# Performance work log

Measured on AMD Instinct MI355X. Metric: run time of the kernel, lower is better.

The kernel has to match this reference:

```python
import jax, jax.numpy as jnp
import numpy as np

B, L = 2, 1024
DIM = 512
N_LAYERS = 2
D_STATE = 16
D_CONV = 4
D_INNER = 2 * DIM          # expand_factor=2
DT_RANK = (DIM + 15) // 16  # ceil(d_model/16) = 32
VOCAB = 32000


def _rmsnorm(x, w, eps=1e-5):
    return x * jax.lax.rsqrt(jnp.mean(x * x, axis=-1, keepdims=True) + eps) * w


def _causal_conv(x, w, b):
    # x: (B,L,D_INNER); depthwise causal conv along L, kernel D_CONV
    xt = jnp.transpose(x, (0, 2, 1))  # (B,C,L)
    y = jax.lax.conv_general_dilated(
        xt, w, window_strides=(1,), padding=[(D_CONV - 1, 0)],
        dimension_numbers=('NCH', 'OIH', 'NCH'), feature_group_count=D_INNER)
    return jnp.transpose(y, (0, 2, 1)) + b


def _ssm(x, xproj_w, dt_w, dt_b, A_log, Dp):
    # x: (B,L,D_INNER)
    A = -jnp.exp(A_log)  # (D_INNER, D_STATE)
    dbc = jnp.einsum('bld,rd->blr', x, xproj_w)  # (B,L,DT_RANK+2*D_STATE)
    delta = jax.nn.softplus(jnp.einsum('blr,dr->bld', dbc[..., :DT_RANK], dt_w) + dt_b)
    Bm = dbc[..., DT_RANK:DT_RANK + D_STATE]   # (B,L,D_STATE)
    Cm = dbc[..., DT_RANK + D_STATE:]          # (B,L,D_STATE)
    dA = jnp.exp(delta[..., None] * A)                       # (B,L,D_INNER,D_STATE)
    dBx = (delta * x)[..., None] * Bm[:, :, None, :]         # (B,L,D_INNER,D_STATE)

    def step(h, inp):
        a, b = inp
        h = a * h + b
        return h, h

    h0 = jnp.zeros((x.shape[0], D_INNER, D_STATE), x.dtype)
    _, hs = jax.lax.scan(step, h0, (jnp.swapaxes(dA, 0, 1), jnp.swapaxes(dBx, 0, 1)))
    y = jnp.einsum('lbds,bls->bld', hs, Cm) + Dp * x
    return y


def _block(h, rw, iw, cw, cb, xw, dw, db, Al, Dp, ow):
    r = _rmsnorm(h, rw)
    xz = jnp.einsum('bld,ed->ble', r, iw)  # (B,L,2*D_INNER)
    xin, z = jnp.split(xz, 2, axis=-1)
    xin = jax.nn.silu(_causal_conv(xin, cw, cb))
    y = _ssm(xin, xw, dw, db, Al, Dp) * jax.nn.silu(z)
    return h + jnp.einsum('ble,de->bld', y, ow)


def _forward(x, embed, rms_w, in_w, conv_w, conv_b, xproj_w, dt_w, dt_b, A_log, Dp, out_w, ln_g, ln_b, head_w, head_b):
    h = embed[x]  # (B,L,DIM)
    for l in range(N_LAYERS):
        h = _block(h, rms_w[l], in_w[l], conv_w[l], conv_b[l], xproj_w[l],
                   dt_w[l], dt_b[l], A_log[l], Dp[l], out_w[l])
    mu = jnp.mean(h, axis=-1, keepdims=True)
    var = jnp.mean((h - mu) ** 2, axis=-1, keepdims=True)
    hn = (h - mu) * jax.lax.rsqrt(var + 1e-5) * ln_g + ln_b
    return jnp.einsum('bld,vd->blv', hn, head_w) + head_b


def setup_inputs() -> dict:
    key = jax.random.key(0)
    ks = jax.random.split(key, 10)
    s = 0.02
    x = jax.random.randint(ks[0], (B, L), 0, VOCAB)
    embed = jax.random.normal(ks[1], (VOCAB, DIM), jnp.float32) * s
    rms_w = jnp.ones((N_LAYERS, DIM), jnp.float32)
    in_w = jax.random.normal(ks[2], (N_LAYERS, 2 * D_INNER, DIM), jnp.float32) * s
    conv_w = jax.random.normal(ks[3], (N_LAYERS, D_INNER, 1, D_CONV), jnp.float32) * s
    conv_b = jnp.zeros((N_LAYERS, D_INNER), jnp.float32)
    xproj_w = jax.random.normal(ks[4], (N_LAYERS, DT_RANK + 2 * D_STATE, D_INNER), jnp.float32) * s
    dt_w = jax.random.normal(ks[5], (N_LAYERS, D_INNER, DT_RANK), jnp.float32) * s
    dt_b = jax.random.normal(ks[6], (N_LAYERS, D_INNER), jnp.float32) * s
    A_log = jnp.log(jnp.broadcast_to(jnp.arange(1, D_STATE + 1, dtype=jnp.float32), (N_LAYERS, D_INNER, D_STATE)))
    Dp = jnp.ones((N_LAYERS, D_INNER), jnp.float32)
    out_w = jax.random.normal(ks[7], (N_LAYERS, DIM, D_INNER), jnp.float32) * s
    ln_g = jnp.ones((DIM,), jnp.float32)
    ln_b = jnp.zeros((DIM,), jnp.float32)
    head_w = jax.random.normal(ks[8], (VOCAB, DIM), jnp.float32) * s
    head_b = jnp.zeros((VOCAB,), jnp.float32)
    return dict(x=x, embed=embed, rms_w=rms_w, in_w=in_w, conv_w=conv_w, conv_b=conv_b,
                xproj_w=xproj_w, dt_w=dt_w, dt_b=dt_b, A_log=A_log, Dp=Dp, out_w=out_w,
                ln_g=ln_g, ln_b=ln_b, head_w=head_w, head_b=head_b)


def reference(x, embed, rms_w, in_w, conv_w, conv_b, xproj_w, dt_w, dt_b, A_log, Dp, out_w, ln_g, ln_b, head_w, head_b):
    return _forward(x, embed, rms_w, in_w, conv_w, conv_b, xproj_w, dt_w, dt_b,
                    A_log, Dp, out_w, ln_g, ln_b, head_w, head_b)
```

## Files before the change

kernel.cpp:

```cpp
#include <hip/hip_runtime.h>

typedef unsigned short u16;
typedef __attribute__((ext_vector_type(8))) __bf16 bf16x8;
typedef __attribute__((ext_vector_type(4))) float f32x4;

#define B_ 2
#define L_ 1024
#define DIM_ 512
#define DINNER_ 1024
#define DSTATE_ 16
#define DTRANK_ 32
#define VOCAB_ 32000
#define NCHUNK 64
#define CLEN 16

__device__ __forceinline__ u16 f2bf(float f) {
    union { float f; unsigned u; } x; x.f = f;
    unsigned r = x.u + 0x7FFFu + ((x.u >> 16) & 1u);
    return (u16)(r >> 16);
}

__global__ __launch_bounds__(256) void prep(const float* __restrict__ in_w,
                                            const float* __restrict__ out_w,
                                            const float* __restrict__ head_w,
                                            const float* __restrict__ dt_w,
                                            const int* __restrict__ x,
                                            const float* __restrict__ embed,
                                            const float* __restrict__ rw,
                                            u16* __restrict__ win,
                                            u16* __restrict__ wout,
                                            u16* __restrict__ whd,
                                            float* __restrict__ dtwT,
                                            float* __restrict__ h,
                                            u16* __restrict__ rbf) {
    int bk = blockIdx.x;
    int t = threadIdx.x;
    if (bk < 19072) {
        const int n1 = 524288;
        const int n2 = n1 + 262144;
        int i = bk * 256 + t;
        const float4* s; ushort4* d; int j;
        if (i < n1)      { s = (const float4*)in_w;   d = (ushort4*)win;  j = i; }
        else if (i < n2) { s = (const float4*)out_w;  d = (ushort4*)wout; j = i - n1; }
        else             { s = (const float4*)head_w; d = (ushort4*)whd;  j = i - n2; }
        float4 v = s[j];
        ushort4 o; o.x = f2bf(v.x); o.y = f2bf(v.y); o.z = f2bf(v.z); o.w = f2bf(v.w);
        d[j] = o;
    } else if (bk < 19328) {
        int bb = bk - 19072;
        int l = bb >> 7;
        int e = (bb & 127) * 256 + t;
        int r = e >> 10, d = e & 1023;
        dtwT[(size_t)l * 32768 + r * 1024 + d] = dt_w[(size_t)l * 32768 + d * 32 + r];
    } else {
        int wave = t >> 6, lane = t & 63;
        int row = (bk - 19328) * 4 + wave;
        int tok = x[row];
        const float4* s = (const float4*)(embed + (size_t)tok * DIM_);
        float4 v0 = s[lane], v1 = s[lane + 64];
        float4* hd = (float4*)(h + (size_t)row * DIM_);
        hd[lane] = v0;
        hd[lane + 64] = v1;
        float ss = v0.x*v0.x + v0.y*v0.y + v0.z*v0.z + v0.w*v0.w
                 + v1.x*v1.x + v1.y*v1.y + v1.z*v1.z + v1.w*v1.w;
        for (int m = 1; m < 64; m <<= 1) ss += __shfl_xor(ss, m);
        float rms = rsqrtf(ss * (1.0f / DIM_) + 1e-5f);
        const float4* w4 = (const float4*)rw;
        float4 w0 = w4[lane], w1 = w4[lane + 64];
        u16* o = rbf + (size_t)row * DIM_;
        ushort4 a, b;
        a.x = f2bf(v0.x * rms * w0.x); a.y = f2bf(v0.y * rms * w0.y);
        a.z = f2bf(v0.z * rms * w0.z); a.w = f2bf(v0.w * rms * w0.w);
        b.x = f2bf(v1.x * rms * w1.x); b.y = f2bf(v1.y * rms * w1.y);
        b.z = f2bf(v1.z * rms * w1.z); b.w = f2bf(v1.w * rms * w1.w);
        *(ushort4*)(o + lane * 4) = a;
        *(ushort4*)(o + 256 + lane * 4) = b;
    }
}

__global__ __launch_bounds__(256) void rmsnorm_bf16(const float* __restrict__ h,
                                                    const float* __restrict__ w,
                                                    u16* __restrict__ out) {
    int wave = threadIdx.x >> 6, lane = threadIdx.x & 63;
    int row = blockIdx.x * 4 + wave;
    const float4* r4 = (const float4*)(h + (size_t)row * DIM_);
    float4 v0 = r4[lane], v1 = r4[lane + 64];
    float ss = v0.x*v0.x + v0.y*v0.y + v0.z*v0.z + v0.w*v0.w
             + v1.x*v1.x + v1.y*v1.y + v1.z*v1.z + v1.w*v1.w;
    for (int m = 1; m < 64; m <<= 1) ss += __shfl_xor(ss, m);
    float rms = rsqrtf(ss * (1.0f / DIM_) + 1e-5f);
    const float4* w4 = (const float4*)w;
    float4 w0 = w4[lane], w1 = w4[lane + 64];
    u16* o = out + (size_t)row * DIM_;
    ushort4 a, b;
    a.x = f2bf(v0.x * rms * w0.x); a.y = f2bf(v0.y * rms * w0.y);
    a.z = f2bf(v0.z * rms * w0.z); a.w = f2bf(v0.w * rms * w0.w);
    b.x = f2bf(v1.x * rms * w1.x); b.y = f2bf(v1.y * rms * w1.y);
    b.z = f2bf(v1.z * rms * w1.z); b.w = f2bf(v1.w * rms * w1.w);
    *(ushort4*)(o + lane * 4) = a;
    *(ushort4*)(o + 256 + lane * 4) = b;
}

__global__ __launch_bounds__(256) void layernorm_bf16(const float* __restrict__ h,
                                                      const float* __restrict__ g,
                                                      const float* __restrict__ bta,
                                                      u16* __restrict__ out) {
    int wave = threadIdx.x >> 6, lane = threadIdx.x & 63;
    int row = blockIdx.x * 4 + wave;
    const float4* r4 = (const float4*)(h + (size_t)row * DIM_);
    float4 v0 = r4[lane], v1 = r4[lane + 64];
    float s = v0.x + v0.y + v0.z + v0.w + v1.x + v1.y + v1.z + v1.w;
    float ss = v0.x*v0.x + v0.y*v0.y + v0.z*v0.z + v0.w*v0.w
             + v1.x*v1.x + v1.y*v1.y + v1.z*v1.z + v1.w*v1.w;
    for (int m = 1; m < 64; m <<= 1) { s += __shfl_xor(s, m); ss += __shfl_xor(ss, m); }
    float mu = s * (1.0f / DIM_);
    float var = ss * (1.0f / DIM_) - mu * mu;
    float rs = rsqrtf(var + 1e-5f);
    const float4* g4 = (const float4*)g;
    const float4* b4 = (const float4*)bta;
    float4 g0 = g4[lane], g1 = g4[lane + 64];
    float4 b0 = b4[lane], b1 = b4[lane + 64];
    u16* o = out + (size_t)row * DIM_;
    ushort4 a, b;
    a.x = f2bf((v0.x - mu) * rs * g0.x + b0.x); a.y = f2bf((v0.y - mu) * rs * g0.y + b0.y);
    a.z = f2bf((v0.z - mu) * rs * g0.z + b0.z); a.w = f2bf((v0.w - mu) * rs * g0.w + b0.w);
    b.x = f2bf((v1.x - mu) * rs * g1.x + b1.x); b.y = f2bf((v1.y - mu) * rs * g1.y + b1.y);
    b.z = f2bf((v1.z - mu) * rs * g1.z + b1.z); b.w = f2bf((v1.w - mu) * rs * g1.w + b1.w);
    *(ushort4*)(o + lane * 4) = a;
    *(ushort4*)(o + 256 + lane * 4) = b;
}

template <int MODE>
__global__ __launch_bounds__(256) void gemm_bt(const u16* __restrict__ A,
                                               const u16* __restrict__ B,
                                               float* __restrict__ C,
                                               const float* __restrict__ bias,
                                               int M, int N, int K,
                                               int nbx, int swzq) {
    __shared__ u16 As[2][128 * 32];
    __shared__ u16 Bs[2][128 * 32];
    const int tid = threadIdx.x;
    const int wave = tid >> 6;
    const int lane = tid & 63;
    int lin = blockIdx.x;
    if (swzq) lin = (lin & 7) * swzq + (lin >> 3);
    const int m0 = (lin % nbx) * 128;
    const int n0 = (lin / nbx) * 128;
    const int wr = wave >> 1, wc = wave & 1;
    f32x4 acc[4][4] = {};

    const int sub = lane >> 2;
    const int koff = (lane & 3) * 8;

    auto stage = [&](int buf, int k0) {
        #pragma unroll
        for (int i = 0; i < 4; ++i) {
            int c = wave * 4 + i;
            const u16* src;
            u16* dst;
            if (c < 8) {
                int row = c * 16 + sub;
                src = A + (size_t)(m0 + row) * K + k0 + koff;
                dst = &As[buf][c * 512];
            } else {
                int cc = c - 8;
                int row = cc * 16 + sub;
                src = B + (size_t)(n0 + row) * K + k0 + koff;
                dst = &Bs[buf][cc * 512];
            }
            __builtin_amdgcn_global_load_lds((const __attribute__((address_space(1))) void*)src,
                                             (__attribute__((address_space(3))) void*)dst,
                                             16, 0, 0);
        }
    };

    const int nt = K / 32;
    stage(0, 0);
    __syncthreads();
    int cur = 0;
    for (int t = 0; t < nt; ++t) {
        if (t + 1 < nt) stage(cur ^ 1, (t + 1) * 32);
        bf16x8 a[4], b[4];
        const int fr = lane & 15;
        const int fk = (lane >> 4) * 8;
        #pragma unroll
        for (int mi = 0; mi < 4; ++mi)
            a[mi] = *(const bf16x8*)(&As[cur][(wr * 64 + mi * 16 + fr) * 32 + fk]);
        #pragma unroll
        for (int ni = 0; ni < 4; ++ni)
            b[ni] = *(const bf16x8*)(&Bs[cur][(wc * 64 + ni * 16 + fr) * 32 + fk]);
        #pragma unroll
        for (int mi = 0; mi < 4; ++mi)
            #pragma unroll
            for (int ni = 0; ni < 4; ++ni)
                acc[mi][ni] = __builtin_amdgcn_mfma_f32_16x16x32_bf16(a[mi], b[ni], acc[mi][ni], 0, 0, 0);
        __syncthreads();
        cur ^= 1;
    }

    const int cl = lane & 15;
    const int rq = (lane >> 4) * 4;
    #pragma unroll
    for (int mi = 0; mi < 4; ++mi) {
        #pragma unroll
        for (int ni = 0; ni < 4; ++ni) {
            int col = n0 + wc * 64 + ni * 16 + cl;
            #pragma unroll
            for (int rr = 0; rr < 4; ++rr) {
                int row = m0 + wr * 64 + mi * 16 + rq + rr;
                size_t idx = (size_t)row * N + col;
                float v = acc[mi][ni][rr];
                if (MODE == 2)      C[idx] = v + bias[col];
                else                C[idx] = v;
            }
        }
    }
}

template <int MODE>
__global__ __launch_bounds__(256) void gemm64(const u16* __restrict__ A,
                                              const u16* __restrict__ B,
                                              float* __restrict__ C,
                                              int M, int N, int K,
                                              int nbx, int swzq) {
    __shared__ u16 As[2][64 * 64];
    __shared__ u16 Bs[2][64 * 64];
    const int tid = threadIdx.x;
    const int wave = tid >> 6;
    const int lane = tid & 63;
    int lin = blockIdx.x;
    if (swzq) lin = (lin & 7) * swzq + (lin >> 3);
    const int m0 = (lin % nbx) * 64;
    const int n0 = (lin / nbx) * 64;
    const int wr = wave >> 1, wc = wave & 1;
    f32x4 acc[2][2] = {};

    const int srow = lane >> 3;
    const int scol = (lane & 7) * 8;

    auto stage = [&](int buf, int k0) {
        #pragma unroll
        for (int i = 0; i < 4; ++i) {
            int c = wave * 4 + i;
            const u16* src;
            u16* dst;
            if (c < 8) {
                int row = c * 8 + srow;
                src = A + (size_t)(m0 + row) * K + k0 + scol;
                dst = &As[buf][c * 512];
            } else {
                int cc = c - 8;
                int row = cc * 8 + srow;
                src = B + (size_t)(n0 + row) * K + k0 + scol;
                dst = &Bs[buf][cc * 512];
            }
            __builtin_amdgcn_global_load_lds((const __attribute__((address_space(1))) void*)src,
                                             (__attribute__((address_space(3))) void*)dst,
                                             16, 0, 0);
        }
    };

    const int nt = K / 64;
    stage(0, 0);
    __syncthreads();
    int cur = 0;
    for (int t = 0; t < nt; ++t) {
        if (t + 1 < nt) stage(cur ^ 1, (t + 1) * 64);
        const int fr = lane & 15;
        const int fk = (lane >> 4) * 8;
        bf16x8 a[2][2], b[2][2];
        #pragma unroll
        for (int ki = 0; ki < 2; ++ki) {
            #pragma unroll
            for (int mi = 0; mi < 2; ++mi)
                a[ki][mi] = *(const bf16x8*)(&As[cur][(wr * 32 + mi * 16 + fr) * 64 + ki * 32 + fk]);
            #pragma unroll
            for (int ni = 0; ni < 2; ++ni)
                b[ki][ni] = *(const bf16x8*)(&Bs[cur][(wc * 32 + ni * 16 + fr) * 64 + ki * 32 + fk]);
        }
        #pragma unroll
        for (int ki = 0; ki < 2; ++ki)
            #pragma unroll
            for (int mi = 0; mi < 2; ++mi)
                #pragma unroll
                for (int ni = 0; ni < 2; ++ni)
                    acc[mi][ni] = __builtin_amdgcn_mfma_f32_16x16x32_bf16(a[ki][mi], b[ki][ni], acc[mi][ni], 0, 0, 0);
        __syncthreads();
        cur ^= 1;
    }

    const int cl = lane & 15;
    const int rq = (lane >> 4) * 4;
    #pragma unroll
    for (int mi = 0; mi < 2; ++mi) {
        #pragma unroll
        for (int ni = 0; ni < 2; ++ni) {
            int col = n0 + wc * 32 + ni * 16 + cl;
            #pragma unroll
            for (int rr = 0; rr < 4; ++rr) {
                int row = m0 + wr * 32 + mi * 16 + rq + rr;
                size_t idx = (size_t)row * N + col;
                float v = acc[mi][ni][rr];
                if (MODE == 1)      C[idx] += v;
                else                C[idx] = v;
            }
        }
    }
}

__global__ __launch_bounds__(256) void conv_xproj_dt(const float* __restrict__ xz,
                                                     const float* __restrict__ cw,
                                                     const float* __restrict__ cb,
                                                     const float* __restrict__ xw,
                                                     const float* __restrict__ dtwT,
                                                     const float* __restrict__ dtb,
                                                     float* __restrict__ xc,
                                                     float* __restrict__ dbc,
                                                     float* __restrict__ delta) {
    __shared__ float sxc[4 * 1024];
    __shared__ float sxw[64 * 132];
    __shared__ float sdbc[4][64];
    int t = threadIdx.x;
    int m0 = blockIdx.x * 4;
    #pragma unroll
    for (int i = 0; i < 16; ++i) {
        int idx = t + i * 256;
        int mi = idx >> 10, d = idx & 1023;
        int m = m0 + mi;
        int l = m & (L_ - 1);
        float acc = cb[d];
        #pragma unroll
        for (int j = 0; j < 4; ++j) {
            int ll = l - 3 + j;
            if (ll >= 0) acc = fmaf(cw[d * 4 + j], xz[(size_t)(m - 3 + j) * (2 * DINNER_) + d], acc);
        }
        float sv = acc / (1.0f + __expf(-acc));
        sxc[mi * 1024 + d] = sv;
        xc[(size_t)m * DINNER_ + d] = sv;
    }
    const int n = t & 63, mi = t >> 6;
    float acc = 0.f;
    for (int kc = 0; kc < 8; ++kc) {
        __syncthreads();
        #pragma unroll
        for (int i = 0; i < 8; ++i) {
            int f = t + i * 256;
            int row = f >> 5, col4 = f & 31;
            float4 v = *(const float4*)(xw + (size_t)row * DINNER_ + kc * 128 + col4 * 4);
            *(float4*)(&sxw[row * 132 + col4 * 4]) = v;
        }
        __syncthreads();
        #pragma unroll
        for (int k4 = 0; k4 < 32; ++k4) {
            float4 wv = *(const float4*)(&sxw[n * 132 + k4 * 4]);
            float4 xv = *(const float4*)(&sxc[mi * 1024 + kc * 128 + k4 * 4]);
            acc += wv.x * xv.x + wv.y * xv.y + wv.z * xv.z + wv.w * xv.w;
        }
    }
    sdbc[mi][n] = acc;
    dbc[(size_t)(m0 + mi) * 64 + n] = acc;
    __syncthreads();
    {
        int d0 = t * 4;
        float4 bias = *(const float4*)(dtb + d0);
        float am[4][4];
        #pragma unroll
        for (int m2 = 0; m2 < 4; ++m2) {
            am[m2][0] = bias.x; am[m2][1] = bias.y; am[m2][2] = bias.z; am[m2][3] = bias.w;
        }
        const float4* wT = (const float4*)dtwT;
        #pragma unroll
        for (int r = 0; r < 32; ++r) {
            float4 wv = wT[r * 256 + t];
            #pragma unroll
            for (int m2 = 0; m2 < 4; ++m2) {
                float s = sdbc[m2][r];
                am[m2][0] = fmaf(s, wv.x, am[m2][0]);
                am[m2][1] = fmaf(s, wv.y, am[m2][1]);
                am[m2][2] = fmaf(s, wv.z, am[m2][2]);
                am[m2][3] = fmaf(s, wv.w, am[m2][3]);
            }
        }
        #pragma unroll
        for (int m2 = 0; m2 < 4; ++m2) {
            float4 o;
            o.x = (am[m2][0] > 20.f) ? am[m2][0] : log1pf(__expf(am[m2][0]));
            o.y = (am[m2][1] > 20.f) ? am[m2][1] : log1pf(__expf(am[m2][1]));
            o.z = (am[m2][2] > 20.f) ? am[m2][2] : log1pf(__expf(am[m2][2]));
            o.w = (am[m2][3] > 20.f) ? am[m2][3] : log1pf(__expf(am[m2][3]));
            *(float4*)(delta + (size_t)(m0 + m2) * DINNER_ + d0) = o;
        }
    }
}

__global__ __launch_bounds__(256) void ssm_part1(const float* __restrict__ delta,
                                                 const float* __restrict__ xc,
                                                 const float* __restrict__ dbc,
                                                 const float* __restrict__ A_log,
                                                 float* __restrict__ hfin,
                                                 float* __restrict__ sumd) {
    int tid = threadIdx.x;
    int d = blockIdx.x * 256 + tid;
    int c = blockIdx.y;
    int b = blockIdx.z;
    __shared__ float sB[CLEN][DSTATE_];
    {
        int l = tid >> 4, s = tid & 15;
        sB[l][s] = dbc[((size_t)(b * L_ + c * CLEN + l)) * 64 + DTRANK_ + s];
    }
    float A[16], h[16];
    {
        const float4* Ar = (const float4*)(A_log + (size_t)d * DSTATE_);
        #pragma unroll
        for (int i = 0; i < 4; ++i) {
            float4 al = Ar[i];
            A[i * 4 + 0] = -__expf(al.x); A[i * 4 + 1] = -__expf(al.y);
            A[i * 4 + 2] = -__expf(al.z); A[i * 4 + 3] = -__expf(al.w);
        }
    }
    #pragma unroll
    for (int s = 0; s < 16; ++s) h[s] = 0.f;
    __syncthreads();
    float sd = 0.f;
    size_t base = ((size_t)b * L_ + c * CLEN) * DINNER_ + d;
    #pragma unroll
    for (int l = 0; l < CLEN; ++l) {
        float dv = delta[base + (size_t)l * DINNER_];
        float xv = xc[base + (size_t)l * DINNER_];
        sd += dv;
        float dx = dv * xv;
        #pragma unroll
        for (int s = 0; s < 16; ++s) {
            float e = __expf(dv * A[s]);
            h[s] = fmaf(e, h[s], dx * sB[l][s]);
        }
    }
    float* hf = hfin + (((size_t)b * NCHUNK + c) * DINNER_ + d) * 16;
    #pragma unroll
    for (int i = 0; i < 4; ++i) {
        float4 v; v.x = h[i*4]; v.y = h[i*4+1]; v.z = h[i*4+2]; v.w = h[i*4+3];
        *(float4*)(hf + i * 4) = v;
    }
    sumd[((size_t)b * NCHUNK + c) * DINNER_ + d] = sd;
}

__global__ __launch_bounds__(256) void ssm_carry(const float* __restrict__ hfin,
                                                 const float* __restrict__ sumd,
                                                 const float* __restrict__ A_log,
                                                 float* __restrict__ h0buf) {
    int t = blockIdx.x * 256 + threadIdx.x;
    int s = t & 15;
    int dg = t >> 4;
    int d = dg & (DINNER_ - 1);
    int b = dg >> 10;
    float As = -__expf(A_log[(size_t)d * DSTATE_ + s]);
    float hc = 0.f;
    #pragma unroll 4
    for (int c = 0; c < NCHUNK; ++c) {
        size_t k = (((size_t)b * NCHUNK + c) * DINNER_ + d) * 16 + s;
        h0buf[k] = hc;
        float sdv = sumd[((size_t)b * NCHUNK + c) * DINNER_ + d];
        float hf = hfin[k];
        hc = fmaf(__expf(As * sdv), hc, hf);
    }
}

__global__ __launch_bounds__(256) void ssm_part2(const float* __restrict__ delta,
                                                 const float* __restrict__ xc,
                                                 const float* __restrict__ dbc,
                                                 const float* __restrict__ xz,
                                                 const float* __restrict__ A_log,
                                                 const float* __restrict__ Dp,
                                                 const float* __restrict__ h0buf,
                                                 u16* __restrict__ ys) {
    int tid = threadIdx.x;
    int d = blockIdx.x * 256 + tid;
    int c = blockIdx.y;
    int b = blockIdx.z;
    __shared__ float sBC[CLEN][32];
    {
        int l = tid >> 5, j = tid & 31;
        sBC[l][j] = dbc[((size_t)(b * L_ + c * CLEN + l)) * 64 + DTRANK_ + j];
        int e1 = tid + 256;
        l = e1 >> 5; j = e1 & 31;
        sBC[l][j] = dbc[((size_t)(b * L_ + c * CLEN + l)) * 64 + DTRANK_ + j];
    }
    float A[16], h[16];
    {
        const float4* Ar = (const float4*)(A_log + (size_t)d * DSTATE_);
        #pragma unroll
        for (int i = 0; i < 4; ++i) {
            float4 al = Ar[i];
            A[i * 4 + 0] = -__expf(al.x); A[i * 4 + 1] = -__expf(al.y);
            A[i * 4 + 2] = -__expf(al.z); A[i * 4 + 3] = -__expf(al.w);
        }
        const float4* h0 = (const float4*)(h0buf + (((size_t)b * NCHUNK + c) * DINNER_ + d) * 16);
        #pragma unroll
        for (int i = 0; i < 4; ++i) {
            float4 v = h0[i];
            h[i * 4 + 0] = v.x; h[i * 4 + 1] = v.y; h[i * 4 + 2] = v.z; h[i * 4 + 3] = v.w;
        }
    }
    float Dval = Dp[d];
    __syncthreads();
    size_t base = ((size_t)b * L_ + c * CLEN) * DINNER_ + d;
    size_t zbase = ((size_t)b * L_ + c * CLEN) * (2 * DINNER_) + DINNER_ + d;
    #pragma unroll
    for (int l = 0; l < CLEN; ++l) {
        float dv = delta[base + (size_t)l * DINNER_];
        float xv = xc[base + (size_t)l * DINNER_];
        float zv = xz[zbase + (size_t)l * (2 * DINNER_)];
        float dx = dv * xv;
        float y = 0.f;
        #pragma unroll
        for (int s = 0; s < 16; ++s) {
            float e = __expf(dv * A[s]);
            h[s] = fmaf(e, h[s], dx * sBC[l][s]);
            y = fmaf(h[s], sBC[l][16 + s], y);
        }
        y = fmaf(Dval, xv, y);
        float sg = zv / (1.0f + __expf(-zv));
        ys[base + (size_t)l * DINNER_] = f2bf(y * sg);
    }
}

extern "C" void kernel_launch(void* const* d_in, const int* in_sizes, int n_in,
                              void* d_out, int out_size, void* d_ws, size_t ws_size,
                              hipStream_t stream) {
    const int*   x       = (const int*)d_in[0];
    const float* embed   = (const float*)d_in[1];
    const float* rms_w   = (const float*)d_in[2];
    const float* in_w    = (const float*)d_in[3];
    const float* conv_w  = (const float*)d_in[4];
    const float* conv_b  = (const float*)d_in[5];
    const float* xproj_w = (const float*)d_in[6];
    const float* dt_w    = (const float*)d_in[7];
    const float* dt_b    = (const float*)d_in[8];
    const float* A_log   = (const float*)d_in[9];
    const float* Dp      = (const float*)d_in[10];
    const float* out_w   = (const float*)d_in[11];
    const float* ln_g    = (const float*)d_in[12];
    const float* ln_b    = (const float*)d_in[13];
    const float* head_w  = (const float*)d_in[14];
    const float* head_b  = (const float*)d_in[15];
    float* out = (float*)d_out;

    char* p = (char*)d_ws;
    auto take = [&](size_t n) { char* q = p; p += (n + 255) & ~(size_t)255; return q; };
    float* h    = (float*)take(2048ull * 512 * 4);
    u16*   r_bf = (u16*)  take(2048ull * 512 * 2);
    float* xz   = (float*)take(2048ull * 2048 * 4);
    float* xc   = (float*)take(2048ull * 1024 * 4);
    float* dbc  = (float*)take(2048ull * 64 * 4);
    float* dlt  = (float*)take(2048ull * 1024 * 4);
    u16*   ys   = (u16*)  take(2048ull * 1024 * 2);
    u16*   hn   = (u16*)  take(2048ull * 512 * 2);
    u16*   win  = (u16*)  take(2ull * 2048 * 512 * 2);
    u16*   wout = (u16*)  take(2ull * 512 * 1024 * 2);
    u16*   whd  = (u16*)  take(32000ull * 512 * 2);
    float* dtwT = (float*)take(2ull * 32 * 1024 * 4);
    float* hfin = (float*)take((size_t)B_ * NCHUNK * DINNER_ * 16 * 4);
    float* h0b  = (float*)take((size_t)B_ * NCHUNK * DINNER_ * 16 * 4);
    float* sumd = (float*)take((size_t)B_ * NCHUNK * DINNER_ * 4);

    prep<<<19840, 256, 0, stream>>>(in_w, out_w, head_w, dt_w, x, embed, rms_w,
                                    win, wout, whd, dtwT, h, r_bf);

    for (int l = 0; l < 2; ++l) {
        if (l > 0) rmsnorm_bf16<<<512, 256, 0, stream>>>(h, rms_w + l * DIM_, r_bf);
        gemm64<0><<<1024, 256, 0, stream>>>(r_bf, win + (size_t)l * 2048 * 512, xz, 2048, 2048, 512, 32, 128);
        conv_xproj_dt<<<512, 256, 0, stream>>>(xz, conv_w + l * DINNER_ * 4, conv_b + l * DINNER_,
                                               xproj_w + (size_t)l * 64 * 1024,
                                               dtwT + (size_t)l * 32 * 1024, dt_b + l * DINNER_,
                                               xc, dbc, dlt);
        ssm_part1<<<dim3(4, NCHUNK, B_), 256, 0, stream>>>(dlt, xc, dbc, A_log + (size_t)l * DINNER_ * DSTATE_, hfin, sumd);
        ssm_carry<<<128, 256, 0, stream>>>(hfin, sumd, A_log + (size_t)l * DINNER_ * DSTATE_, h0b);
        ssm_part2<<<dim3(4, NCHUNK, B_), 256, 0, stream>>>(dlt, xc, dbc, xz, A_log + (size_t)l * DINNER_ * DSTATE_,
                                                           Dp + l * DINNER_, h0b, ys);
        gemm64<1><<<256, 256, 0, stream>>>(ys, wout + (size_t)l * 512 * 1024, h, 2048, 512, 1024, 32, 32);
    }

    layernorm_bf16<<<512, 256, 0, stream>>>(h, ln_g, ln_b, hn);
    gemm_bt<2><<<4000, 256, 0, stream>>>(hn, whd, out, head_b, 2048, VOCAB_, 512, 16, 500);
}
```

Before: 404.1 us.

## Swizzle GEMM LDS layout, deepen K-tile, retile conv/xproj to 8 rows

The 128x128 head GEMM now stages 64-wide K tiles instead of 32, and both GEMM kernels use an XOR-swizzled LDS column layout to avoid bank conflicts on fragment loads. The in-projection switches from the 64x64 GEMM to the 128x128 kernel with fewer blocks. The conv/xproj/dt kernel processes 8 rows per block, splits the K reduction across waves and sums the partials in shared memory, so each weight tile is reused across more rows. In exchange it uses more LDS and registers per block and launches fewer blocks, which can lower occupancy.

```diff
diff --git a/kernel.cpp b/kernel.cpp
--- a/kernel.cpp
+++ b/kernel.cpp
@@ -137,8 +137,8 @@
                                                const float* __restrict__ bias,
                                                int M, int N, int K,
                                                int nbx, int swzq) {
-    __shared__ u16 As[2][128 * 32];
-    __shared__ u16 Bs[2][128 * 32];
+    __shared__ u16 As[2][128 * 64];
+    __shared__ u16 Bs[2][128 * 64];
     const int tid = threadIdx.x;
     const int wave = tid >> 6;
     const int lane = tid & 63;
@@ -149,23 +149,23 @@
     const int wr = wave >> 1, wc = wave & 1;
     f32x4 acc[4][4] = {};
 
-    const int sub = lane >> 2;
-    const int koff = (lane & 3) * 8;
+    const int crow = lane >> 3;
+    const int scol = ((lane & 7) ^ crow) * 8;
 
     auto stage = [&](int buf, int k0) {
         #pragma unroll
-        for (int i = 0; i < 4; ++i) {
-            int c = wave * 4 + i;
+        for (int i = 0; i < 8; ++i) {
+            int c = wave * 8 + i;
             const u16* src;
             u16* dst;
-            if (c < 8) {
-                int row = c * 16 + sub;
-                src = A + (size_t)(m0 + row) * K + k0 + koff;
+            if (c < 16) {
+                int row = c * 8 + crow;
+                src = A + (size_t)(m0 + row) * K + k0 + scol;
                 dst = &As[buf][c * 512];
             } else {
-                int cc = c - 8;
-                int row = cc * 16 + sub;
-                src = B + (size_t)(n0 + row) * K + k0 + koff;
+                int cc = c - 16;
+                int row = cc * 8 + crow;
+                src = B + (size_t)(n0 + row) * K + k0 + scol;
                 dst = &Bs[buf][cc * 512];
             }
             __builtin_amdgcn_global_load_lds((const __attribute__((address_space(1))) void*)src,
@@ -174,26 +174,35 @@
         }
     };
 
-    const int nt = K / 32;
+    const int nt = K / 64;
     stage(0, 0);
     __syncthreads();
     int cur = 0;
+    const int fr = lane & 15;
+    const int q = lane >> 4;
     for (int t = 0; t < nt; ++t) {
-        if (t + 1 < nt) stage(cur ^ 1, (t + 1) * 32);
-        bf16x8 a[4], b[4];
-        const int fr = lane & 15;
-        const int fk = (lane >> 4) * 8;
-        #pragma unroll
-        for (int mi = 0; mi < 4; ++mi)
-            a[mi] = *(const bf16x8*)(&As[cur][(wr * 64 + mi * 16 + fr) * 32 + fk]);
-        #pragma unroll
-        for (int ni = 0; ni < 4; ++ni)
-            b[ni] = *(const bf16x8*)(&Bs[cur][(wc * 64 + ni * 16 + fr) * 32 + fk]);
-        #pragma unroll
-        for (int mi = 0; mi < 4; ++mi)
-            #pragma unroll
-            for (int ni = 0; ni < 4; ++ni)
-                acc[mi][ni] = __builtin_amdgcn_mfma_f32_16x16x32_bf16(a[mi], b[ni], acc[mi][ni], 0, 0, 0);
+        if (t + 1 < nt) stage(cur ^ 1, (t + 1) * 64);
+        bf16x8 a[2][4], b[2][4];
+        #pragma unroll
+        for (int ki = 0; ki < 2; ++ki) {
+            #pragma unroll
+            for (int mi = 0; mi < 4; ++mi) {
+                int row = wr * 64 + mi * 16 + fr;
+                a[ki][mi] = *(const bf16x8*)(&As[cur][row * 64 + ((((ki << 2) + q) ^ (fr & 7)) * 8)]);
+            }
+            #pragma unroll
+            for (int ni = 0; ni < 4; ++ni) {
+                int row = wc * 64 + ni * 16 + fr;
+                b[ki][ni] = *(const bf16x8*)(&Bs[cur][row * 64 + ((((ki << 2) + q) ^ (fr & 7)) * 8)]);
+            }
+        }
+        #pragma unroll
+        for (int ki = 0; ki < 2; ++ki)
+            #pragma unroll
+            for (int mi = 0; mi < 4; ++mi)
+                #pragma unroll
+                for (int ni = 0; ni < 4; ++ni)
+                    acc[mi][ni] = __builtin_amdgcn_mfma_f32_16x16x32_bf16(a[ki][mi], b[ki][ni], acc[mi][ni], 0, 0, 0);
         __syncthreads();
         cur ^= 1;
     }
@@ -235,8 +244,8 @@
     const int wr = wave >> 1, wc = wave & 1;
     f32x4 acc[2][2] = {};
 
-    const int srow = lane >> 3;
-    const int scol = (lane & 7) * 8;
+    const int crow = lane >> 3;
+    const int scol = ((lane & 7) ^ crow) * 8;
 
     auto stage = [&](int buf, int k0) {
         #pragma unroll
@@ -245,12 +254,12 @@
             const u16* src;
             u16* dst;
             if (c < 8) {
-                int row = c * 8 + srow;
+                int row = c * 8 + crow;
                 src = A + (size_t)(m0 + row) * K + k0 + scol;
                 dst = &As[buf][c * 512];
             } else {
                 int cc = c - 8;
-                int row = cc * 8 + srow;
+                int row = cc * 8 + crow;
                 src = B + (size_t)(n0 + row) * K + k0 + scol;
                 dst = &Bs[buf][cc * 512];
             }
@@ -264,19 +273,23 @@
     stage(0, 0);
     __syncthreads();
     int cur = 0;
+    const int fr = lane & 15;
+    const int q = lane >> 4;
     for (int t = 0; t < nt; ++t) {
         if (t + 1 < nt) stage(cur ^ 1, (t + 1) * 64);
-        const int fr = lane & 15;
-        const int fk = (lane >> 4) * 8;
         bf16x8 a[2][2], b[2][2];
         #pragma unroll
         for (int ki = 0; ki < 2; ++ki) {
             #pragma unroll
-            for (int mi = 0; mi < 2; ++mi)
-                a[ki][mi] = *(const bf16x8*)(&As[cur][(wr * 32 + mi * 16 + fr) * 64 + ki * 32 + fk]);
-            #pragma unroll
-            for (int ni = 0; ni < 2; ++ni)
-                b[ki][ni] = *(const bf16x8*)(&Bs[cur][(wc * 32 + ni * 16 + fr) * 64 + ki * 32 + fk]);
+            for (int mi = 0; mi < 2; ++mi) {
+                int row = wr * 32 + mi * 16 + fr;
+                a[ki][mi] = *(const bf16x8*)(&As[cur][row * 64 + ((((ki << 2) + q) ^ (fr & 7)) * 8)]);
+            }
+            #pragma unroll
+            for (int ni = 0; ni < 2; ++ni) {
+                int row = wc * 32 + ni * 16 + fr;
+                b[ki][ni] = *(const bf16x8*)(&Bs[cur][row * 64 + ((((ki << 2) + q) ^ (fr & 7)) * 8)]);
+            }
         }
         #pragma unroll
         for (int ki = 0; ki < 2; ++ki)
@@ -317,13 +330,14 @@
                                                      float* __restrict__ xc,
                                                      float* __restrict__ dbc,
                                                      float* __restrict__ delta) {
-    __shared__ float sxc[4 * 1024];
+    __shared__ float sxc[8 * 1024];
     __shared__ float sxw[64 * 132];
-    __shared__ float sdbc[4][64];
+    __shared__ float sred[4][8][68];
+    __shared__ float sdbc[8][64];
     int t = threadIdx.x;
-    int m0 = blockIdx.x * 4;
-    #pragma unroll
-    for (int i = 0; i < 16; ++i) {
+    int m0 = blockIdx.x * 8;
+    #pragma unroll
+    for (int i = 0; i < 32; ++i) {
         int idx = t + i * 256;
         int mi = idx >> 10, d = idx & 1023;
         int m = m0 + mi;
@@ -338,57 +352,68 @@
         sxc[mi * 1024 + d] = sv;
         xc[(size_t)m * DINNER_ + d] = sv;
     }
-    const int n = t & 63, mi = t >> 6;
-    float acc = 0.f;
+    const int n = t & 63, kg = t >> 6;
+    float acc8[8] = {};
     for (int kc = 0; kc < 8; ++kc) {
         __syncthreads();
         #pragma unroll
         for (int i = 0; i < 8; ++i) {
             int f = t + i * 256;
             int row = f >> 5, col4 = f & 31;
-            float4 v = *(const float4*)(xw + (size_t)row * DINNER_ + kc * 128 + col4 * 4);
-            *(float4*)(&sxw[row * 132 + col4 * 4]) = v;
+            *(float4*)(&sxw[row * 132 + col4 * 4]) =
+                *(const float4*)(xw + (size_t)row * DINNER_ + kc * 128 + col4 * 4);
         }
         __syncthreads();
         #pragma unroll
-        for (int k4 = 0; k4 < 32; ++k4) {
+        for (int k4i = 0; k4i < 8; ++k4i) {
+            int k4 = kg * 8 + k4i;
             float4 wv = *(const float4*)(&sxw[n * 132 + k4 * 4]);
-            float4 xv = *(const float4*)(&sxc[mi * 1024 + kc * 128 + k4 * 4]);
-            acc += wv.x * xv.x + wv.y * xv.y + wv.z * xv.z + wv.w * xv.w;
-        }
-    }
-    sdbc[mi][n] = acc;
-    dbc[(size_t)(m0 + mi) * 64 + n] = acc;
+            #pragma unroll
+            for (int mi = 0; mi < 8; ++mi) {
+                float4 xv = *(const float4*)(&sxc[mi * 1024 + kc * 128 + k4 * 4]);
+                acc8[mi] += wv.x * xv.x + wv.y * xv.y + wv.z * xv.z + wv.w * xv.w;
+            }
+        }
+    }
+    #pragma unroll
+    for (int mi = 0; mi < 8; ++mi) sred[kg][mi][n] = acc8[mi];
+    __syncthreads();
+    #pragma unroll
+    for (int rep = 0; rep < 2; ++rep) {
+        int o = t + rep * 256;
+        int mi = o >> 6, n2 = o & 63;
+        float v = sred[0][mi][n2] + sred[1][mi][n2] + sred[2][mi][n2] + sred[3][mi][n2];
+        sdbc[mi][n2] = v;
+        dbc[(size_t)(m0 + mi) * 64 + n2] = v;
+    }
     __syncthreads();
     {
         int d0 = t * 4;
         float4 bias = *(const float4*)(dtb + d0);
-        float am[4][4];
-        #pragma unroll
-        for (int m2 = 0; m2 < 4; ++m2) {
-            am[m2][0] = bias.x; am[m2][1] = bias.y; am[m2][2] = bias.z; am[m2][3] = bias.w;
-        }
+        float4 am[8];
+        #pragma unroll
+        for (int mi = 0; mi < 8; ++mi) am[mi] = bias;
         const float4* wT = (const float4*)dtwT;
         #pragma unroll
         for (int r = 0; r < 32; ++r) {
             float4 wv = wT[r * 256 + t];
             #pragma unroll
-            for (int m2 = 0; m2 < 4; ++m2) {
-                float s = sdbc[m2][r];
-                am[m2][0] = fmaf(s, wv.x, am[m2][0]);
-                am[m2][1] = fmaf(s, wv.y, am[m2][1]);
-                am[m2][2] = fmaf(s, wv.z, am[m2][2]);
-                am[m2][3] = fmaf(s, wv.w, am[m2][3]);
-            }
-        }
-        #pragma unroll
-        for (int m2 = 0; m2 < 4; ++m2) {
+            for (int mi = 0; mi < 8; ++mi) {
+                float s = sdbc[mi][r];
+                am[mi].x = fmaf(s, wv.x, am[mi].x);
+                am[mi].y = fmaf(s, wv.y, am[mi].y);
+                am[mi].z = fmaf(s, wv.z, am[mi].z);
+                am[mi].w = fmaf(s, wv.w, am[mi].w);
+            }
+        }
+        #pragma unroll
+        for (int mi = 0; mi < 8; ++mi) {
             float4 o;
-            o.x = (am[m2][0] > 20.f) ? am[m2][0] : log1pf(__expf(am[m2][0]));
-            o.y = (am[m2][1] > 20.f) ? am[m2][1] : log1pf(__expf(am[m2][1]));
-            o.z = (am[m2][2] > 20.f) ? am[m2][2] : log1pf(__expf(am[m2][2]));
-            o.w = (am[m2][3] > 20.f) ? am[m2][3] : log1pf(__expf(am[m2][3]));
-            *(float4*)(delta + (size_t)(m0 + m2) * DINNER_ + d0) = o;
+            o.x = (am[mi].x > 20.f) ? am[mi].x : log1pf(__expf(am[mi].x));
+            o.y = (am[mi].y > 20.f) ? am[mi].y : log1pf(__expf(am[mi].y));
+            o.z = (am[mi].z > 20.f) ? am[mi].z : log1pf(__expf(am[mi].z));
+            o.w = (am[mi].w > 20.f) ? am[mi].w : log1pf(__expf(am[mi].w));
+            *(float4*)(delta + (size_t)(m0 + mi) * DINNER_ + d0) = o;
         }
     }
 }
@@ -568,8 +593,8 @@
 
     for (int l = 0; l < 2; ++l) {
         if (l > 0) rmsnorm_bf16<<<512, 256, 0, stream>>>(h, rms_w + l * DIM_, r_bf);
-        gemm64<0><<<1024, 256, 0, stream>>>(r_bf, win + (size_t)l * 2048 * 512, xz, 2048, 2048, 512, 32, 128);
-        conv_xproj_dt<<<512, 256, 0, stream>>>(xz, conv_w + l * DINNER_ * 4, conv_b + l * DINNER_,
+        gemm_bt<0><<<256, 256, 0, stream>>>(r_bf, win + (size_t)l * 2048 * 512, xz, nullptr, 2048, 2048, 512, 16, 32);
+        conv_xproj_dt<<<256, 256, 0, stream>>>(xz, conv_w + l * DINNER_ * 4, conv_b + l * DINNER_,
                                                xproj_w + (size_t)l * 64 * 1024,
                                                dtwT + (size_t)l * 32 * 1024, dt_b + l * DINNER_,
                                                xc, dbc, dlt);
```

Result: faster. 378.3 us (-6.4%).
